# Performance work log

Measured on AMD Instinct MI355X. Metric: run time of the kernel, lower is better.

The kernel has to match this reference:

```python
import jax, jax.numpy as jnp
import numpy as np
from jax import lax

B, L, D_MODEL = 2, 2048, 768
D_STATE, D_INNER, DT_RANK, K = 16, 1536, 48, 4


def setup_inputs() -> dict:
    key = jax.random.key(0)
    ks = jax.random.split(key, 10)
    x = jax.random.normal(ks[0], (B, L, D_MODEL), dtype=jnp.float32)
    in_proj_w = 0.02 * jax.random.normal(ks[1], (2 * D_INNER, D_MODEL), dtype=jnp.float32)
    conv_w = 0.1 * jax.random.normal(ks[2], (D_INNER, 1, K), dtype=jnp.float32)
    conv_b = 0.01 * jax.random.normal(ks[3], (D_INNER,), dtype=jnp.float32)
    # A_log initialized as log(1..d_state) per channel (as in _init_parameters)
    A_log = jnp.tile(jnp.log(jnp.arange(1, D_STATE + 1, dtype=jnp.float32)), (D_INNER, 1))
    D_param = jnp.ones((D_INNER,), dtype=jnp.float32)
    x_proj_w = 0.02 * jax.random.normal(ks[4], (DT_RANK + 2 * D_STATE, D_INNER), dtype=jnp.float32)
    dt_proj_w = jax.random.uniform(ks[5], (D_INNER, DT_RANK), minval=-0.1, maxval=0.1, dtype=jnp.float32)
    dt_proj_b = 0.01 * jax.random.normal(ks[6], (D_INNER,), dtype=jnp.float32)
    out_proj_w = 0.02 * jax.random.normal(ks[7], (D_MODEL, D_INNER), dtype=jnp.float32)
    return {"x": x, "in_proj_w": in_proj_w, "conv_w": conv_w, "conv_b": conv_b,
            "A_log": A_log, "D_param": D_param, "x_proj_w": x_proj_w,
            "dt_proj_w": dt_proj_w, "dt_proj_b": dt_proj_b, "out_proj_w": out_proj_w}


def _forward(x, in_proj_w, conv_w, conv_b, A_log, D_param, x_proj_w, dt_proj_w, dt_proj_b, out_proj_w):
    xz = jnp.einsum('bld,ed->ble', x, in_proj_w)            # [B,L,2*d_inner]
    xp, z = jnp.split(xz, 2, axis=-1)                        # [B,L,d_inner] each
    # depthwise causal conv1d: torch Conv1d(padding=3)[..., :L] == left-pad 3, valid conv
    xc = lax.conv_general_dilated(
        xp.transpose(0, 2, 1), conv_w, window_strides=(1,),
        padding=[(K - 1, 0)], feature_group_count=D_INNER)   # [B,d_inner,L]
    xc = (xc + conv_b[None, :, None]).transpose(0, 2, 1)     # [B,L,d_inner]
    xc = jax.nn.silu(xc)
    x_dbl = jnp.einsum('bld,ed->ble', xc, x_proj_w)          # [B,L,dt_rank+2*d_state]
    dt_low, Bmat, Cmat = jnp.split(x_dbl, [DT_RANK, DT_RANK + D_STATE], axis=-1)
    dt = jax.nn.softplus(jnp.einsum('blr,dr->bld', dt_low, dt_proj_w) + dt_proj_b)  # [B,L,d_inner]
    A = -jnp.exp(A_log)                                      # [d_inner,d_state]
    A_bar = jnp.exp(dt[..., None] * A[None, None])           # [B,L,d_inner,d_state]
    Bx = (dt * xc)[..., None] * Bmat[:, :, None, :]          # [B,L,d_inner,d_state]
    # time-major scan over the recurrence h = A_bar*h + B_bar*x
    A_t = A_bar.transpose(1, 0, 2, 3)
    Bx_t = Bx.transpose(1, 0, 2, 3)
    C_t = Cmat.transpose(1, 0, 2)                            # [L,B,d_state]
    h0 = jnp.zeros((B, D_INNER, D_STATE), dtype=x.dtype)

    def step(h, inp):
        a, bx, c = inp
        h = a * h + bx
        y = jnp.einsum('bds,bs->bd', h, c)
        return h, y

    _, ys = lax.scan(step, h0, (A_t, Bx_t, C_t))             # ys: [L,B,d_inner]
    y = ys.transpose(1, 0, 2)
    y = y + xc * D_param
    y = y * jax.nn.silu(z)
    return jnp.einsum('bld,md->blm', y, out_proj_w)          # [B,L,d_model]


def reference(x, in_proj_w, conv_w, conv_b, A_log, D_param, x_proj_w, dt_proj_w, dt_proj_b, out_proj_w):
    return _forward(x, in_proj_w, conv_w, conv_b, A_log, D_param, x_proj_w, dt_proj_w, dt_proj_b, out_proj_w)
```

## Files before the change

kernel.cpp:

```cpp
#include <hip/hip_runtime.h>
#include <stdint.h>

#define B_SZ    2
#define L_SEQ   2048
#define DMODEL  768
#define DSTATE  16
#define DINNER  1536
#define DTRANK  48
#define M_ROWS  4096
#define NSEG    4
#define SEGL    512
#define NSC     16
#define SCL     32
#define KSPLIT  8

typedef __attribute__((ext_vector_type(8))) short bf16x8;
typedef __attribute__((ext_vector_type(4))) float f32x4;
typedef __attribute__((ext_vector_type(2))) float f32x2;
typedef __attribute__((ext_vector_type(4))) unsigned int u32x4;
typedef __attribute__((ext_vector_type(2))) unsigned int u32x2;

__device__ __forceinline__ unsigned short f2bf(float f) {
  unsigned int u = __float_as_uint(f);
  u += 0x7FFFu + ((u >> 16) & 1u);
  return (unsigned short)(u >> 16);
}
__device__ __forceinline__ unsigned int pack2bf(float a, float b) {
  return (unsigned int)f2bf(a) | ((unsigned int)f2bf(b) << 16);
}
__device__ __forceinline__ float bf2f(unsigned short h) {
  return __uint_as_float(((unsigned int)h) << 16);
}
__device__ __forceinline__ float fexp(float x) {
  return __builtin_amdgcn_exp2f(x * 1.44269504088896340736f);
}
__device__ __forceinline__ float sigm(float x) {
  return 1.0f / (1.0f + fexp(-x));
}

template <int CTRL>
__device__ __forceinline__ float dpp_add(float v) {
  int x = __builtin_amdgcn_update_dpp(0, __float_as_int(v), CTRL, 0xF, 0xF, true);
  return v + __int_as_float(x);
}
__device__ __forceinline__ float quad_sum(float v) {
  v = dpp_add<0xB1>(v);
  v = dpp_add<0x4E>(v);
  return v;
}
__device__ __forceinline__ float row16_sum(float v) {
  v = dpp_add<0xB1>(v);
  v = dpp_add<0x4E>(v);
  v = dpp_add<0x124>(v);
  v = dpp_add<0x128>(v);
  return v;
}

__global__ void cast_all_kernel(const float* __restrict__ x, const float* __restrict__ w1,
                                const float* __restrict__ w2, const float* __restrict__ w3,
                                const float* __restrict__ dtw,
                                unsigned short* __restrict__ xbf, unsigned short* __restrict__ w1bf,
                                unsigned short* __restrict__ w2bf, unsigned short* __restrict__ w3bf,
                                unsigned short* __restrict__ dtwbf) {
  int i = blockIdx.x * 256 + threadIdx.x;
  const int n_x = M_ROWS * DMODEL;
  const int n_w1 = 2 * DINNER * DMODEL;
  const int n_w3 = DMODEL * DINNER;
  const int n_w2 = 128 * DINNER;
  const int n_dtw = DINNER * 64;
  if (i < n_x)  { xbf[i] = f2bf(x[i]); return; }  i -= n_x;
  if (i < n_w1) { w1bf[i] = f2bf(w1[i]); return; } i -= n_w1;
  if (i < n_w3) { w3bf[i] = f2bf(w3[i]); return; } i -= n_w3;
  if (i < n_w2) {
    int row = i / DINNER, col = i - row * DINNER;
    w2bf[i] = (row < (DTRANK + 2 * DSTATE)) ? f2bf(w2[row * DINNER + col]) : (unsigned short)0;
    return;
  }
  i -= n_w2;
  if (i < n_dtw) {
    int row = i >> 6, col = i & 63;
    dtwbf[i] = (col < DTRANK) ? f2bf(dtw[row * DTRANK + col]) : (unsigned short)0;
  }
}

__global__ void xdbl_pack_kernel(const float* __restrict__ xdblS,
                                 unsigned short* __restrict__ dtlbf,
                                 float* __restrict__ BCt) {
  const int SLAB = M_ROWS * 128;
  int i = blockIdx.x * 256 + threadIdx.x;
  const int n_dtl = M_ROWS * 64;
  if (i < n_dtl) {
    int row = i >> 6, col = i & 63;
    if (col < DTRANK) {
      float v = 0.f;
#pragma unroll
      for (int z = 0; z < KSPLIT; z++) v += xdblS[(size_t)z * SLAB + row * 128 + col];
      dtlbf[i] = f2bf(v);
    } else dtlbf[i] = 0;
    return;
  }
  i -= n_dtl;
  int l4 = i & 511;
  int j  = (i >> 9) & 31;
  int b  = (i >> 14) & 1;
  f32x4 o;
#pragma unroll
  for (int k = 0; k < 4; k++) {
    float v = 0.f;
    size_t base = ((size_t)b * L_SEQ + l4 * 4 + k) * 128 + DTRANK + j;
#pragma unroll
    for (int z = 0; z < KSPLIT; z++) v += xdblS[(size_t)z * SLAB + base];
    o[k] = v;
  }
  *(f32x4*)(BCt + ((size_t)b * 32 + j) * L_SEQ + l4 * 4) = o;
}

template <int EPI>
__global__ __launch_bounds__(256, 2) void gemm_bt(
    const unsigned short* __restrict__ A, const unsigned short* __restrict__ Bt,
    float* __restrict__ C, int K, int KS, int ldc, long slab,
    const float* __restrict__ bias) {
  __shared__ unsigned short As[128 * 40];
  __shared__ unsigned short Bs[128 * 40];
  const int tid = threadIdx.x;
  const int m0 = blockIdx.x * 128;
  const int n0 = blockIdx.y * 128;
  const int ks = blockIdx.z * KS, ke = ks + KS;
  float* Cz = C + (size_t)blockIdx.z * slab;
  const int lane = tid & 63;
  const int wave = tid >> 6;
  const int wr = (wave >> 1) * 64, wc = (wave & 1) * 64;
  const int lm = lane & 15, q = lane >> 4;
  const int r = tid >> 2, sg = (tid & 3) * 8;

  f32x4 acc[4][4] = {};

  for (int k0 = ks; k0 < ke; k0 += 32) {
    u32x4 a0 = *(const u32x4*)(A + (size_t)(m0 + r) * K + k0 + sg);
    u32x4 a1 = *(const u32x4*)(A + (size_t)(m0 + r + 64) * K + k0 + sg);
    u32x4 b0 = *(const u32x4*)(Bt + (size_t)(n0 + r) * K + k0 + sg);
    u32x4 b1 = *(const u32x4*)(Bt + (size_t)(n0 + r + 64) * K + k0 + sg);
    __syncthreads();
    *(u32x4*)&As[r * 40 + sg] = a0;
    *(u32x4*)&As[(r + 64) * 40 + sg] = a1;
    *(u32x4*)&Bs[r * 40 + sg] = b0;
    *(u32x4*)&Bs[(r + 64) * 40 + sg] = b1;
    __syncthreads();
    bf16x8 af[4], bq[4];
#pragma unroll
    for (int mt = 0; mt < 4; mt++)
      af[mt] = *(const bf16x8*)&As[(wr + mt * 16 + lm) * 40 + q * 8];
#pragma unroll
    for (int nt = 0; nt < 4; nt++)
      bq[nt] = *(const bf16x8*)&Bs[(wc + nt * 16 + lm) * 40 + q * 8];
#pragma unroll
    for (int mt = 0; mt < 4; mt++)
#pragma unroll
      for (int nt = 0; nt < 4; nt++)
        acc[mt][nt] = __builtin_amdgcn_mfma_f32_16x16x32_bf16(af[mt], bq[nt], acc[mt][nt], 0, 0, 0);
  }

#pragma unroll
  for (int mt = 0; mt < 4; mt++) {
    int row0 = m0 + wr + mt * 16 + q * 4;
    float bs4[4];
    if (EPI == 2) {
#pragma unroll
      for (int i = 0; i < 4; i++) bs4[i] = bias[row0 + i];
    }
#pragma unroll
    for (int nt = 0; nt < 4; nt++) {
      int col = n0 + wc + nt * 16 + lm;
#pragma unroll
      for (int i = 0; i < 4; i++) {
        float v = acc[mt][nt][i];
        if (EPI == 2) {
          v += bs4[i];
          v = (v > 15.f) ? v : log1pf(fexp(v));
        }
        Cz[(size_t)(row0 + i) * ldc + col] = v;
      }
    }
  }
}

__global__ __launch_bounds__(256) void conv_silu_t(const float* __restrict__ xz,
                                                   const float* __restrict__ cw,
                                                   const float* __restrict__ cb,
                                                   unsigned short* __restrict__ xcbf,
                                                   unsigned short* __restrict__ xcT) {
  __shared__ float tl[67 * 68];
  __shared__ unsigned short xs[64 * 80];
  __shared__ float cws[64 * 4];
  __shared__ float cbs[64];
  const int r0 = blockIdx.x * 64;
  const int c0 = blockIdx.y * 64;
  const int t = threadIdx.x;
  cws[t] = cw[(c0 + (t >> 2)) * 4 + (t & 3)];
  if (t < 64) cbs[t] = cb[c0 + t];
  const bool lowedge = (r0 & (L_SEQ - 1)) == 0;
#pragma unroll
  for (int it = 0; it < 5; it++) {
    int idx = t + it * 256;
    int rr = idx >> 4;
    int cs4 = (idx & 15) * 4;
    if (rr < 67) {
      f32x4 v;
      if (lowedge && rr < 3) v = (f32x4){0.f, 0.f, 0.f, 0.f};
      else v = *(const f32x4*)(xz + (size_t)(r0 + rr - 3) * 3072 + c0 + cs4);
      *(f32x4*)&tl[rr * 68 + cs4] = v;
    }
  }
  __syncthreads();
  const int cs = (t & 15) * 4;
  f32x4 w0, w1, w2, w3, cbv;
#pragma unroll
  for (int j = 0; j < 4; j++) {
    w0[j] = cws[(cs + j) * 4 + 0];
    w1[j] = cws[(cs + j) * 4 + 1];
    w2[j] = cws[(cs + j) * 4 + 2];
    w3[j] = cws[(cs + j) * 4 + 3];
    cbv[j] = cbs[cs + j];
  }
#pragma unroll
  for (int it = 0; it < 4; it++) {
    int r = (t >> 4) + it * 16;
    f32x4 t0 = *(const f32x4*)&tl[(r + 0) * 68 + cs];
    f32x4 t1 = *(const f32x4*)&tl[(r + 1) * 68 + cs];
    f32x4 t2 = *(const f32x4*)&tl[(r + 2) * 68 + cs];
    f32x4 t3 = *(const f32x4*)&tl[(r + 3) * 68 + cs];
    f32x4 acc = cbv + w0 * t0 + w1 * t1 + w2 * t2 + w3 * t3;
#pragma unroll
    for (int j = 0; j < 4; j++) acc[j] = acc[j] * sigm(acc[j]);
    u32x2 pk;
    pk[0] = pack2bf(acc[0], acc[1]);
    pk[1] = pack2bf(acc[2], acc[3]);
    *(u32x2*)(xcbf + (size_t)(r0 + r) * DINNER + c0 + cs) = pk;
    *(u32x2*)&xs[r * 80 + cs] = pk;
  }
  __syncthreads();
#pragma unroll
  for (int it = 0; it < 2; it++) {
    int idx = t + it * 256;
    int cc = idx & 63, rs = idx >> 6;
    unsigned int w[4];
#pragma unroll
    for (int p = 0; p < 4; p++) {
      unsigned int lo = xs[(rs * 8 + 2 * p) * 80 + cc];
      unsigned int hi = xs[(rs * 8 + 2 * p + 1) * 80 + cc];
      w[p] = lo | (hi << 16);
    }
    *(u32x4*)(xcT + (size_t)(c0 + cc) * M_ROWS + r0 + rs * 8) = *(u32x4*)w;
  }
}

__global__ __launch_bounds__(256) void transpose_silu(const float* __restrict__ xz,
                                                      unsigned short* __restrict__ out) {
  __shared__ float tl[64 * 68];
  const int r0 = blockIdx.x * 64;
  const int c0 = blockIdx.y * 64;
  const int tid = threadIdx.x;
#pragma unroll
  for (int it = 0; it < 4; it++) {
    int idx = tid + it * 256;
    int rr = idx >> 4, cs = idx & 15;
    f32x4 v = *(const f32x4*)(xz + (size_t)(r0 + rr) * 3072 + DINNER + c0 + cs * 4);
#pragma unroll
    for (int p = 0; p < 4; p++) v[p] = v[p] * sigm(v[p]);
    *(f32x4*)&tl[rr * 68 + cs * 4] = v;
  }
  __syncthreads();
#pragma unroll
  for (int it = 0; it < 2; it++) {
    int idx = tid + it * 256;
    int cc = idx & 63, rs = idx >> 6;
    unsigned int w[4];
#pragma unroll
    for (int p = 0; p < 4; p++)
      w[p] = pack2bf(tl[(rs * 8 + 2 * p) * 68 + cc], tl[(rs * 8 + 2 * p + 1) * 68 + cc]);
    *(u32x4*)(out + (size_t)(c0 + cc) * M_ROWS + r0 + rs * 8) = *(u32x4*)w;
  }
}

struct SC32 { f32x2 dt; unsigned int xc, sz; f32x4 B0, B1, C0, C1; };

template <int FULL>
__global__ __launch_bounds__(64) void scan_seg(
    const float* __restrict__ dtT, const unsigned short* __restrict__ xcT,
    const float* __restrict__ BCt, const unsigned short* __restrict__ szT,
    const float* __restrict__ A_log, const float* __restrict__ Dp,
    const float* __restrict__ HIN, float* __restrict__ P, float* __restrict__ HL,
    unsigned short* __restrict__ ybf) {
  __shared__ float dtS[2][4 * 36];
  __shared__ float dtxS[2][4 * 36];
  __shared__ float BS[2][16 * 36];
  __shared__ float CS[2][16 * 36];
  __shared__ unsigned int xcR[2][4 * 18];
  __shared__ unsigned int szR[2][4 * 18];
  __shared__ float ysh[16 * 36];
  const int lane = threadIdx.x;
  const int s = lane & 15, dl = lane >> 4;
  const int d0 = blockIdx.x * 4;
  const int d = d0 + dl;
  const int b = blockIdx.y;
  const int seg = blockIdx.z;
  const int lseg = seg * SEGL;
  const size_t rbase = (size_t)b * L_SEQ + lseg;
  const float a2 = -fexp(A_log[d * 16 + s]) * 1.44269504f;
  const float dpv = Dp[d];
  const float* dtbase = dtT + (size_t)d0 * M_ROWS + rbase;
  const unsigned short* xcbase = xcT + (size_t)d0 * M_ROWS + rbase;
  const unsigned short* szbase = szT + (size_t)d0 * M_ROWS + rbase;
  const float* Bbase = BCt + (size_t)b * 32 * L_SEQ + lseg;
  const float* Cbase = Bbase + 16 * L_SEQ;
  const int ch = lane >> 4, li = lane & 15;
  const int s4 = lane >> 2, lj = lane & 3;
  float* ywp = &ysh[(dl * 4 + (s >> 2)) * 36 + (s & 3)];
  const bool sb0 = (s & 1) != 0, sb1 = (s & 2) != 0;
  float h = 0.f, sdt = 0.f;
  size_t o = (((size_t)seg * B_SZ + b) * DINNER + d) * 16 + s;
  if (FULL) h = HIN[o];

  auto load32 = [&](SC32& R, int l0) {
    R.dt = *(const f32x2*)(dtbase + (size_t)ch * M_ROWS + l0 + li * 2);
    R.xc = *(const unsigned int*)(xcbase + (size_t)ch * M_ROWS + l0 + li * 2);
    if (FULL) R.sz = *(const unsigned int*)(szbase + (size_t)ch * M_ROWS + l0 + li * 2);
    R.B0 = *(const f32x4*)(Bbase + (size_t)s4 * L_SEQ + l0 + lj * 8);
    R.B1 = *(const f32x4*)(Bbase + (size_t)s4 * L_SEQ + l0 + lj * 8 + 4);
    if (FULL) {
      R.C0 = *(const f32x4*)(Cbase + (size_t)s4 * L_SEQ + l0 + lj * 8);
      R.C1 = *(const f32x4*)(Cbase + (size_t)s4 * L_SEQ + l0 + lj * 8 + 4);
    }
  };
  auto store32 = [&](int p, const SC32& R) {
    if (!FULL) sdt += R.dt[0] + R.dt[1];
    f32x2 xf, dtx;
    xf[0] = __uint_as_float(R.xc << 16);
    xf[1] = __uint_as_float(R.xc & 0xFFFF0000u);
    dtx = R.dt * xf;
    *(f32x2*)&dtS[p][ch * 36 + li * 2] = R.dt;
    *(f32x2*)&dtxS[p][ch * 36 + li * 2] = dtx;
    if (FULL) {
      xcR[p][ch * 18 + li] = R.xc;
      szR[p][ch * 18 + li] = R.sz;
    }
    *(f32x4*)&BS[p][s4 * 36 + lj * 8] = R.B0;
    *(f32x4*)&BS[p][s4 * 36 + lj * 8 + 4] = R.B1;
    if (FULL) {
      *(f32x4*)&CS[p][s4 * 36 + lj * 8] = R.C0;
      *(f32x4*)&CS[p][s4 * 36 + lj * 8 + 4] = R.C1;
    }
  };

  SC32 R;
  load32(R, 0);
  store32(0, R);
  load32(R, SCL);

#pragma unroll 1
  for (int c = 0; c < NSC; c++) {
    const int p = c & 1;
#pragma unroll
    for (int g = 0; g < 4; g++) {
      const int l0g = g * 8;
      f32x4 dta = *(const f32x4*)&dtS[p][dl * 36 + l0g];
      f32x4 dtb = *(const f32x4*)&dtS[p][dl * 36 + l0g + 4];
      f32x4 xa  = *(const f32x4*)&dtxS[p][dl * 36 + l0g];
      f32x4 xb  = *(const f32x4*)&dtxS[p][dl * 36 + l0g + 4];
      f32x4 Ba  = *(const f32x4*)&BS[p][s * 36 + l0g];
      f32x4 Bb  = *(const f32x4*)&BS[p][s * 36 + l0g + 4];
      f32x4 Ca, Cb;
      if (FULL) {
        Ca = *(const f32x4*)&CS[p][s * 36 + l0g];
        Cb = *(const f32x4*)&CS[p][s * 36 + l0g + 4];
      }
      float p8[8];
#pragma unroll
      for (int j = 0; j < 8; j++) {
        float dtj = (j < 4) ? dta[j] : dtb[j - 4];
        float dxj = (j < 4) ? xa[j]  : xb[j - 4];
        float Bj  = (j < 4) ? Ba[j]  : Bb[j - 4];
        float a = __builtin_amdgcn_exp2f(dtj * a2);
        h = a * h + dxj * Bj;
        if (FULL) {
          float Cj = (j < 4) ? Ca[j] : Cb[j - 4];
          p8[j] = h * Cj;
        }
      }
      if (FULL) {
#pragma unroll
        for (int half = 0; half < 2; half++) {
          float q0 = quad_sum(p8[half * 4 + 0]);
          float q1 = quad_sum(p8[half * 4 + 1]);
          float q2 = quad_sum(p8[half * 4 + 2]);
          float q3 = quad_sum(p8[half * 4 + 3]);
          float v01 = sb0 ? q1 : q0;
          float v23 = sb0 ? q3 : q2;
          ywp[g * 8 + half * 4] = sb1 ? v23 : v01;
        }
      }
    }
    if (FULL) {
      f32x2 y0 = *(const f32x2*)&ysh[(dl * 4 + 0) * 36 + s * 2];
      f32x2 y1 = *(const f32x2*)&ysh[(dl * 4 + 1) * 36 + s * 2];
      f32x2 y2 = *(const f32x2*)&ysh[(dl * 4 + 2) * 36 + s * 2];
      f32x2 y3 = *(const f32x2*)&ysh[(dl * 4 + 3) * 36 + s * 2];
      f32x2 ys = y0 + y1 + y2 + y3;
      unsigned int xcu = xcR[p][dl * 18 + s];
      unsigned int szu = szR[p][dl * 18 + s];
      float xcf[2] = {__uint_as_float(xcu << 16), __uint_as_float(xcu & 0xFFFF0000u)};
      float szf[2] = {__uint_as_float(szu << 16), __uint_as_float(szu & 0xFFFF0000u)};
      size_t rr0 = rbase + c * SCL + s * 2;
#pragma unroll
      for (int i = 0; i < 2; i++) {
        float yv = ys[i] + xcf[i] * dpv;
        ybf[(rr0 + i) * DINNER + d] = f2bf(yv * szf[i]);
      }
    }
    if (c < NSC - 1) {
      store32(p ^ 1, R);
      if (c < NSC - 2) load32(R, (c + 2) * SCL);
    }
  }
  if (!FULL) {
    sdt = row16_sum(sdt);
    P[o] = __builtin_amdgcn_exp2f(a2 * sdt);
    HL[o] = h;
  }
}

__global__ void scan_comb(const float* __restrict__ P, const float* __restrict__ HL,
                          float* __restrict__ HIN) {
  int tg = blockIdx.x * 256 + threadIdx.x;
  int s = tg & 15;
  int rem = tg >> 4;
  int d = rem % DINNER;
  int b = rem / DINNER;
  float h = 0.f;
  for (int g = 0; g < NSEG; g++) {
    size_t o = (((size_t)g * B_SZ + b) * DINNER + d) * 16 + s;
    HIN[o] = h;
    if (g < NSEG - 1) h = P[o] * h + HL[o];
  }
}

extern "C" void kernel_launch(void* const* d_in, const int* in_sizes, int n_in,
                              void* d_out, int out_size, void* d_ws, size_t ws_size,
                              hipStream_t stream) {
  const float* x    = (const float*)d_in[0];
  const float* w1   = (const float*)d_in[1];
  const float* cw   = (const float*)d_in[2];
  const float* cb   = (const float*)d_in[3];
  const float* alog = (const float*)d_in[4];
  const float* Dp   = (const float*)d_in[5];
  const float* w2   = (const float*)d_in[6];
  const float* dtw  = (const float*)d_in[7];
  const float* dtb  = (const float*)d_in[8];
  const float* w3   = (const float*)d_in[9];
  float* out = (float*)d_out;
  char* ws = (char*)d_ws;

  size_t off = 0;
  auto alloc = [&](size_t bytes) { size_t o = off; off += (bytes + 255) & ~(size_t)255; return o; };
  char*           xzr   = ws + alloc((size_t)M_ROWS * 3072 * 4);
  float*          xz    = (float*)xzr;
  float*          dtT   = (float*)xzr;
  unsigned short* ybf   = (unsigned short*)(xzr + (size_t)DINNER * M_ROWS * 4);
  float*          xdblS = (float*)(ws + alloc((size_t)KSPLIT * M_ROWS * 128 * 4));
  unsigned short* xbf   = (unsigned short*)(ws + alloc((size_t)M_ROWS * DMODEL * 2));
  unsigned short* w1bf  = (unsigned short*)(ws + alloc((size_t)2 * DINNER * DMODEL * 2));
  unsigned short* w2bf  = (unsigned short*)(ws + alloc((size_t)128 * DINNER * 2));
  unsigned short* w3bf  = (unsigned short*)(ws + alloc((size_t)DMODEL * DINNER * 2));
  unsigned short* dtlbf = (unsigned short*)(ws + alloc((size_t)M_ROWS * 64 * 2));
  unsigned short* dtwbf = (unsigned short*)(ws + alloc((size_t)DINNER * 64 * 2));
  unsigned short* xcbf  = (unsigned short*)(ws + alloc((size_t)M_ROWS * DINNER * 2));
  unsigned short* xcT   = (unsigned short*)(ws + alloc((size_t)DINNER * M_ROWS * 2));
  unsigned short* szbf  = (unsigned short*)(ws + alloc((size_t)DINNER * M_ROWS * 2));
  float*          BCt   = (float*)(ws + alloc((size_t)B_SZ * 32 * L_SEQ * 4));
  float*          Pbuf  = (float*)(ws + alloc((size_t)NSEG * B_SZ * DINNER * 16 * 4));
  float*          HLbuf = (float*)(ws + alloc((size_t)NSEG * B_SZ * DINNER * 16 * 4));
  float*          HINb  = (float*)(ws + alloc((size_t)NSEG * B_SZ * DINNER * 16 * 4));

  cast_all_kernel<<<27264, 256, 0, stream>>>(x, w1, w2, w3, dtw, xbf, w1bf, w2bf, w3bf, dtwbf);
  gemm_bt<0><<<dim3(32, 24), 256, 0, stream>>>(xbf, w1bf, xz, DMODEL, DMODEL, 3072, 0, nullptr);
  conv_silu_t<<<dim3(64, 24), 256, 0, stream>>>(xz, cw, cb, xcbf, xcT);
  transpose_silu<<<dim3(64, 24), 256, 0, stream>>>(xz, szbf);
  gemm_bt<0><<<dim3(32, 1, KSPLIT), 256, 0, stream>>>(xcbf, w2bf, xdblS, DINNER,
                                                      DINNER / KSPLIT, 128,
                                                      (long)M_ROWS * 128, nullptr);
  xdbl_pack_kernel<<<1152, 256, 0, stream>>>(xdblS, dtlbf, BCt);
  gemm_bt<2><<<dim3(12, 32), 256, 0, stream>>>(dtwbf, dtlbf, dtT, 64, 64, M_ROWS, 0, dtb);
  scan_seg<0><<<dim3(384, 2, NSEG - 1), 64, 0, stream>>>(dtT, xcT, BCt, szbf, alog, Dp,
                                                         nullptr, Pbuf, HLbuf, nullptr);
  scan_comb<<<192, 256, 0, stream>>>(Pbuf, HLbuf, HINb);
  scan_seg<1><<<dim3(384, 2, NSEG), 64, 0, stream>>>(dtT, xcT, BCt, szbf, alog, Dp,
                                                     HINb, nullptr, nullptr, ybf);
  gemm_bt<0><<<dim3(32, 6), 256, 0, stream>>>(ybf, w3bf, out, DINNER, DINNER, 768, 0, nullptr);
}
```

Baseline: 314.6 us.

## Double scan segments and drop register/LDS prefetch double-buffering in scan

Raises the number of chunked-scan segments from 4 to 8 (segment length 256), doubling the blocks in the scan kernels and halving the serial chain each block walks. It also removes the double-buffered LDS staging and the one-chunk-ahead register prefetch, so each chunk is loaded then consumed directly, and sizes the C/y/xc/sz buffers to one element in the non-FULL variant. The aim is more parallelism and lower LDS and register use for better occupancy, at the cost of exposed global load latency per chunk and extra work in the combine pass. There are no barriers between the LDS writes and reads, so this relies on the block being a single 64-lane wavefront.

Measured after the change: 304.6 us. 1.03x faster.

```diff
diff --git a/kernel.cpp b/kernel.cpp
--- a/kernel.cpp
+++ b/kernel.cpp
@@ -8,9 +8,9 @@
 #define DINNER  1536
 #define DTRANK  48
 #define M_ROWS  4096
-#define NSEG    4
-#define SEGL    512
-#define NSC     16
+#define NSEG    8
+#define SEGL    256
+#define NSC     8
 #define SCL     32
 #define KSPLIT  8
 
@@ -291,13 +291,13 @@
     const float* __restrict__ A_log, const float* __restrict__ Dp,
     const float* __restrict__ HIN, float* __restrict__ P, float* __restrict__ HL,
     unsigned short* __restrict__ ybf) {
-  __shared__ float dtS[2][4 * 36];
-  __shared__ float dtxS[2][4 * 36];
-  __shared__ float BS[2][16 * 36];
-  __shared__ float CS[2][16 * 36];
-  __shared__ unsigned int xcR[2][4 * 18];
-  __shared__ unsigned int szR[2][4 * 18];
-  __shared__ float ysh[16 * 36];
+  __shared__ float dtS[4 * 36];
+  __shared__ float dtxS[4 * 36];
+  __shared__ float BS[16 * 36];
+  __shared__ float CS[FULL ? 16 * 36 : 1];
+  __shared__ unsigned int xcR[FULL ? 4 * 18 : 1];
+  __shared__ unsigned int szR[FULL ? 4 * 18 : 1];
+  __shared__ float ysh[FULL ? 16 * 36 : 1];
   const int lane = threadIdx.x;
   const int s = lane & 15, dl = lane >> 4;
   const int d0 = blockIdx.x * 4;
@@ -332,47 +332,44 @@
       R.C1 = *(const f32x4*)(Cbase + (size_t)s4 * L_SEQ + l0 + lj * 8 + 4);
     }
   };
-  auto store32 = [&](int p, const SC32& R) {
+  auto store32 = [&](const SC32& R) {
     if (!FULL) sdt += R.dt[0] + R.dt[1];
     f32x2 xf, dtx;
     xf[0] = __uint_as_float(R.xc << 16);
     xf[1] = __uint_as_float(R.xc & 0xFFFF0000u);
     dtx = R.dt * xf;
-    *(f32x2*)&dtS[p][ch * 36 + li * 2] = R.dt;
-    *(f32x2*)&dtxS[p][ch * 36 + li * 2] = dtx;
+    *(f32x2*)&dtS[ch * 36 + li * 2] = R.dt;
+    *(f32x2*)&dtxS[ch * 36 + li * 2] = dtx;
     if (FULL) {
-      xcR[p][ch * 18 + li] = R.xc;
-      szR[p][ch * 18 + li] = R.sz;
-    }
-    *(f32x4*)&BS[p][s4 * 36 + lj * 8] = R.B0;
-    *(f32x4*)&BS[p][s4 * 36 + lj * 8 + 4] = R.B1;
+      xcR[ch * 18 + li] = R.xc;
+      szR[ch * 18 + li] = R.sz;
+    }
+    *(f32x4*)&BS[s4 * 36 + lj * 8] = R.B0;
+    *(f32x4*)&BS[s4 * 36 + lj * 8 + 4] = R.B1;
     if (FULL) {
-      *(f32x4*)&CS[p][s4 * 36 + lj * 8] = R.C0;
-      *(f32x4*)&CS[p][s4 * 36 + lj * 8 + 4] = R.C1;
+      *(f32x4*)&CS[s4 * 36 + lj * 8] = R.C0;
+      *(f32x4*)&CS[s4 * 36 + lj * 8 + 4] = R.C1;
     }
   };
-
-  SC32 R;
-  load32(R, 0);
-  store32(0, R);
-  load32(R, SCL);
 
 #pragma unroll 1
   for (int c = 0; c < NSC; c++) {
-    const int p = c & 1;
+    SC32 R;
+    load32(R, c * SCL);
+    store32(R);
 #pragma unroll
     for (int g = 0; g < 4; g++) {
       const int l0g = g * 8;
-      f32x4 dta = *(const f32x4*)&dtS[p][dl * 36 + l0g];
-      f32x4 dtb = *(const f32x4*)&dtS[p][dl * 36 + l0g + 4];
-      f32x4 xa  = *(const f32x4*)&dtxS[p][dl * 36 + l0g];
-      f32x4 xb  = *(const f32x4*)&dtxS[p][dl * 36 + l0g + 4];
-      f32x4 Ba  = *(const f32x4*)&BS[p][s * 36 + l0g];
-      f32x4 Bb  = *(const f32x4*)&BS[p][s * 36 + l0g + 4];
+      f32x4 dta = *(const f32x4*)&dtS[dl * 36 + l0g];
+      f32x4 dtb = *(const f32x4*)&dtS[dl * 36 + l0g + 4];
+      f32x4 xa  = *(const f32x4*)&dtxS[dl * 36 + l0g];
+      f32x4 xb  = *(const f32x4*)&dtxS[dl * 36 + l0g + 4];
+      f32x4 Ba  = *(const f32x4*)&BS[s * 36 + l0g];
+      f32x4 Bb  = *(const f32x4*)&BS[s * 36 + l0g + 4];
       f32x4 Ca, Cb;
       if (FULL) {
-        Ca = *(const f32x4*)&CS[p][s * 36 + l0g];
-        Cb = *(const f32x4*)&CS[p][s * 36 + l0g + 4];
+        Ca = *(const f32x4*)&CS[s * 36 + l0g];
+        Cb = *(const f32x4*)&CS[s * 36 + l0g + 4];
       }
       float p8[8];
 #pragma unroll
@@ -406,8 +403,8 @@
       f32x2 y2 = *(const f32x2*)&ysh[(dl * 4 + 2) * 36 + s * 2];
       f32x2 y3 = *(const f32x2*)&ysh[(dl * 4 + 3) * 36 + s * 2];
       f32x2 ys = y0 + y1 + y2 + y3;
-      unsigned int xcu = xcR[p][dl * 18 + s];
-      unsigned int szu = szR[p][dl * 18 + s];
+      unsigned int xcu = xcR[dl * 18 + s];
+      unsigned int szu = szR[dl * 18 + s];
       float xcf[2] = {__uint_as_float(xcu << 16), __uint_as_float(xcu & 0xFFFF0000u)};
       float szf[2] = {__uint_as_float(szu << 16), __uint_as_float(szu & 0xFFFF0000u)};
       size_t rr0 = rbase + c * SCL + s * 2;
@@ -416,10 +413,6 @@
         float yv = ys[i] + xcf[i] * dpv;
         ybf[(rr0 + i) * DINNER + d] = f2bf(yv * szf[i]);
       }
-    }
-    if (c < NSC - 1) {
-      store32(p ^ 1, R);
-      if (c < NSC - 2) load32(R, (c + 2) * SCL);
     }
   }
   if (!FULL) {
```
